# Performance work log

Hardware: AMD Instinct MI355X
Metric: run time of the kernel (lower is better)

The kernel has to match this reference:

```python
import jax, jax.numpy as jnp
import numpy as np

B, T, C = 2, 2048, 1024
H = 16
D = C // H  # 64
SCALE = 1.0 / np.sqrt(D)


def setup_inputs() -> dict:
    key = jax.random.key(0)
    k1, k2, k3 = jax.random.split(key, 3)
    x = jax.random.normal(k1, (B, T, C), dtype=jnp.float32)
    Wqkv = jax.random.normal(k2, (C, 3 * C), dtype=jnp.float32) * 0.02
    bqkv = jnp.zeros((3 * C,), dtype=jnp.float32)
    Wo = jax.random.normal(k3, (C, C), dtype=jnp.float32) * 0.02
    bo = jnp.zeros((C,), dtype=jnp.float32)
    return {"x": x, "Wqkv": Wqkv, "bqkv": bqkv, "Wo": Wo, "bo": bo}


def reference(x, Wqkv, bqkv, Wo, bo):
    Bsz, Tlen, Cdim = x.shape
    qkv = x @ Wqkv + bqkv                       # [B,T,3C]
    qkv = qkv.reshape(Bsz, Tlen, 3, H, D)
    qkv = jnp.transpose(qkv, (2, 0, 3, 1, 4))   # [3,B,H,T,D]
    q, k, v = qkv[0], qkv[1], qkv[2]
    att = jnp.einsum("bhqd,bhkd->bhqk", q, k) * SCALE
    # NOTE: faithful to source: mask keeps positions where k >= q
    i = jnp.arange(Tlen)
    mask = i[None, :] >= i[:, None]             # [T,T], entry [q,k]: k >= q
    att = jnp.where(mask[None, None], att, -jnp.inf)
    att = jax.nn.softmax(att, axis=-1)
    # dropout p=0.0 (inference) -> identity
    y = jnp.einsum("bhqk,bhkd->bhqd", att, v)   # [B,H,T,D]
    y = jnp.transpose(y, (0, 2, 1, 3)).reshape(Bsz, Tlen, Cdim)
    y = y @ Wo + bo
    return y
```

## Files before the change

kernel.cpp:

```cpp
#include <hip/hip_runtime.h>
#include <hip/hip_bf16.h>
#include <cstdint>
#include <cstddef>

typedef __bf16 bf16_t;
typedef __bf16 bf16x8 __attribute__((ext_vector_type(8)));
typedef __bf16 bf16x4 __attribute__((ext_vector_type(4)));
typedef short short4v __attribute__((ext_vector_type(4)));
typedef float f32x4 __attribute__((ext_vector_type(4)));

#define NB 2
#define NT 2048
#define NC 1024
#define NH 16
#define ND 64
#define NM (NB * NT)
#define N3 (3 * NC)
#define QSCALE_LOG2E 0.18033688011112042f

#define GLOAD_LDS16(gptr, lptr)                                                          \
  __builtin_amdgcn_global_load_lds((const __attribute__((address_space(1))) void*)(gptr), \
                                   (__attribute__((address_space(3))) void*)(lptr), 16, 0, 0)

__global__ __launch_bounds__(256) void prep_k(const float* __restrict__ x,
                                              const float* __restrict__ Wqkv,
                                              const float* __restrict__ Wo,
                                              bf16_t* __restrict__ xbf,
                                              bf16_t* __restrict__ wqkvT,
                                              bf16_t* __restrict__ woT) {
  __shared__ float tile[32][33];
  const int bx = blockIdx.x;
  if (bx < 4096) {
    const int i = (bx * 256 + threadIdx.x) * 4;
    const float4 v = *(const float4*)(x + i);
    bf16x4 o;
    o[0] = (bf16_t)v.x; o[1] = (bf16_t)v.y; o[2] = (bf16_t)v.z; o[3] = (bf16_t)v.w;
    *(bf16x4*)(xbf + i) = o;
    return;
  }
  const int t = bx - 4096;
  const int cxi = t & 127;
  const int tr = (t >> 7) * 32;
  const float* in;
  bf16_t* out;
  int Ccols, tc;
  if (cxi < 96) { in = Wqkv; out = wqkvT; Ccols = 3072; tc = cxi * 32; }
  else          { in = Wo;   out = woT;   Ccols = 1024; tc = (cxi - 96) * 32; }
  const int lx = threadIdx.x & 31;
  const int ly = threadIdx.x >> 5;
#pragma unroll
  for (int i = 0; i < 32; i += 8)
    tile[ly + i][lx] = in[(size_t)(tr + ly + i) * Ccols + tc + lx];
  __syncthreads();
#pragma unroll
  for (int i = 0; i < 32; i += 8)
    out[(size_t)(tc + ly + i) * 1024 + tr + lx] = (bf16_t)tile[lx][ly + i];
}

__global__ __launch_bounds__(256) void qkv_gemm_k(const bf16_t* __restrict__ A,
                                                  const bf16_t* __restrict__ Bt,
                                                  const float* __restrict__ bias,
                                                  bf16_t* __restrict__ qb,
                                                  bf16_t* __restrict__ kb,
                                                  bf16_t* __restrict__ vt2) {
  __shared__ __align__(16) bf16_t As0[4096], Bs0[4096], As1[4096], Bs1[4096];
  const int xcd = blockIdx.x & 7;
  const int i2 = blockIdx.x >> 3;
  const int m0 = (i2 & 31) * 128;
  const int n0 = (xcd * 3 + (i2 >> 5)) * 128;

  const int lane = threadIdx.x & 63;
  const int w = threadIdx.x >> 6;
  const int wm = (w & 1) * 64, wn = (w >> 1) * 64;
  const int quad = lane >> 4, l16 = lane & 15;

  f32x4 acc[4][4] = {};

  auto stage = [&](int k0, bf16_t* As_, bf16_t* Bs_) {
#pragma unroll
    for (int i = 0; i < 2; ++i) {
      const int gb = w * 128 + i * 64;
      const int g = gb + lane;
      GLOAD_LDS16(A + (size_t)(m0 + (g >> 2)) * NC + k0 + (g & 3) * 8, As_ + gb * 8);
      GLOAD_LDS16(Bt + (size_t)(n0 + (g >> 2)) * NC + k0 + (g & 3) * 8, Bs_ + gb * 8);
    }
  };

  auto compute = [&](const bf16_t* As_, const bf16_t* Bs_) {
    bf16x8 af[4], bfr[4];
#pragma unroll
    for (int i = 0; i < 4; ++i)
      af[i] = *(const bf16x8*)(As_ + (wm + i * 16 + l16) * 32 + quad * 8);
#pragma unroll
    for (int j = 0; j < 4; ++j)
      bfr[j] = *(const bf16x8*)(Bs_ + (wn + j * 16 + l16) * 32 + quad * 8);
#pragma unroll
    for (int i = 0; i < 4; ++i)
#pragma unroll
      for (int j = 0; j < 4; ++j)
        acc[i][j] = __builtin_amdgcn_mfma_f32_16x16x32_bf16(af[i], bfr[j], acc[i][j], 0, 0, 0);
  };

  stage(0, As0, Bs0);
  int k0 = 0;
  while (true) {
    __syncthreads();
    if (k0 + 32 < NC) stage(k0 + 32, As1, Bs1);
    compute(As0, Bs0);
    k0 += 32; if (k0 >= NC) break;
    __syncthreads();
    if (k0 + 32 < NC) stage(k0 + 32, As0, Bs0);
    compute(As1, Bs1);
    k0 += 32; if (k0 >= NC) break;
  }

#pragma unroll
  for (int i = 0; i < 4; ++i)
#pragma unroll
    for (int j = 0; j < 4; ++j) {
      const int n = n0 + wn + j * 16 + l16;
      const float bn = bias[n];
      const int which = n >> 10;
      const int rem = n & 1023;
      const int h = rem >> 6, d = rem & 63;
      const int mb = m0 + wm + i * 16 + quad * 4;
      const int b = mb >> 11, t4 = mb & 2047;
      const size_t bh = (size_t)b * NH + h;
      if (which == 2) {
        const int c = t4 >> 6, g = (t4 >> 2) & 15;
        bf16x4 val;
#pragma unroll
        for (int r = 0; r < 4; ++r) val[r] = (bf16_t)(acc[i][j][r] + bn);
        *(bf16x4*)(vt2 + ((bh * 32 + c) * 1024 + (size_t)g * 64 + d) * 4) = val;
      } else {
        bf16_t* dst = (which == 0) ? qb : kb;
        const float sc = (which == 0) ? QSCALE_LOG2E : 1.0f;
#pragma unroll
        for (int r = 0; r < 4; ++r)
          dst[(bh * NT + t4 + r) * ND + d] = (bf16_t)((acc[i][j][r] + bn) * sc);
      }
    }
}

__global__ __launch_bounds__(256, 4) void attn_k(const bf16_t* __restrict__ q,
                                                 const bf16_t* __restrict__ k,
                                                 const bf16_t* __restrict__ vt2,
                                                 bf16_t* __restrict__ y ) {
  const int bh = blockIdx.x & 31;
  const int u = (blockIdx.x >> 5) & 7;
  const int r4 = blockIdx.x >> 8;
  const int T = r4 * 8 + ((r4 & 1) ? (7 - u) : u);
  const int b = bh >> 4, h = bh & 15;

  const bf16_t* qp = q + (size_t)bh * NT * ND;
  const bf16_t* kp = k + (size_t)bh * NT * ND;
  const bf16_t* vp = vt2 + (size_t)bh * 32 * 4096;

  __shared__ __align__(16) bf16_t kbuf0[4096], kbuf1[4096];
  __shared__ __align__(16) bf16_t vbuf0[4096], vbuf1[4096];

  const int lane = threadIdx.x & 63;
  const int w = threadIdx.x >> 6;
  const int quad = lane >> 4, l16 = lane & 15;
  const int qv = T * 64 + w * 16 + l16;

  const bf16x8 qf0 = *(const bf16x8*)(qp + (size_t)qv * ND + quad * 8);
  const bf16x8 qf1 = *(const bf16x8*)(qp + (size_t)qv * ND + 32 + quad * 8);

  const short4v ones = {0x3F80, 0x3F80, 0x3F80, 0x3F80};

  f32x4 zs = {0.f, 0.f, 0.f, 0.f};
  f32x4 o[4];
#pragma unroll
  for (int dj = 0; dj < 4; ++dj) o[dj] = (f32x4){0.f, 0.f, 0.f, 0.f};

  auto stage = [&](int c, bf16_t* kb_, bf16_t* vb_) {
    const bf16_t* kc = kp + (size_t)c * 4096;
    const bf16_t* vc = vp + (size_t)c * 4096;
#pragma unroll
    for (int i = 0; i < 2; ++i) {
      const int gb = w * 128 + i * 64;
      const int s = gb + lane;
      const int row = s >> 3;
      const int cs = (s & 7) ^ (row & 7);
      GLOAD_LDS16(kc + (size_t)row * 64 + cs * 8, kb_ + gb * 8);
      GLOAD_LDS16(vc + (size_t)s * 8, vb_ + gb * 8);
    }
  };

  auto step = [&](const bf16_t* kt, const bf16_t* vt, int c) {
    const int t0 = c * 64;
    f32x4 sv[4];
#pragma unroll
    for (int kj = 0; kj < 4; ++kj) {
      const int kr = kj * 16 + l16;
      const int sw = kr & 7;
      const bf16x8 a0 = *(const bf16x8*)(kt + ((size_t)kr * 8 + (quad ^ sw)) * 8);
      const bf16x8 a1 = *(const bf16x8*)(kt + ((size_t)kr * 8 + ((4 + quad) ^ sw)) * 8);
      f32x4 z = {0.f, 0.f, 0.f, 0.f};
      z = __builtin_amdgcn_mfma_f32_16x16x32_bf16(a0, qf0, z, 0, 0, 0);
      z = __builtin_amdgcn_mfma_f32_16x16x32_bf16(a1, qf1, z, 0, 0, 0);
      sv[kj] = z;
    }
    if (c == T) {
#pragma unroll
      for (int kj = 0; kj < 4; ++kj)
#pragma unroll
        for (int r = 0; r < 4; ++r)
          if (t0 + kj * 16 + quad * 4 + r < qv) sv[kj][r] = -INFINITY;
    }
    short4v pf[4];
#pragma unroll
    for (int kj = 0; kj < 4; ++kj) {
      bf16x4 pb;
#pragma unroll
      for (int r = 0; r < 4; ++r) pb[r] = (bf16_t)__builtin_amdgcn_exp2f(sv[kj][r]);
      pf[kj] = __builtin_bit_cast(short4v, pb);
    }
#pragma unroll
    for (int kj = 0; kj < 4; ++kj)
      zs = __builtin_amdgcn_mfma_f32_16x16x16bf16_1k(ones, pf[kj], zs, 0, 0, 0);
#pragma unroll
    for (int dj = 0; dj < 4; ++dj) {
#pragma unroll
      for (int kj = 0; kj < 4; ++kj) {
        const bf16x4 a =
            *(const bf16x4*)(vt + ((size_t)(kj * 4 + quad) * 64 + dj * 16 + l16) * 4);
        o[dj] = __builtin_amdgcn_mfma_f32_16x16x16bf16_1k(
            __builtin_bit_cast(short4v, a), pf[kj], o[dj], 0, 0, 0);
      }
    }
  };

  stage(T, kbuf0, vbuf0);
  int c = T;
  while (true) {
    __syncthreads();
    if (c + 1 < 32) stage(c + 1, kbuf1, vbuf1);
    step(kbuf0, vbuf0, c);
    if (++c >= 32) break;
    __syncthreads();
    if (c + 1 < 32) stage(c + 1, kbuf0, vbuf0);
    step(kbuf1, vbuf1, c);
    if (++c >= 32) break;
  }

  const float inv = 1.0f / zs[0];
  const size_t base = ((size_t)b * NT + qv) * NC + h * 64;
#pragma unroll
  for (int dj = 0; dj < 4; ++dj) {
    bf16x4 va;
#pragma unroll
    for (int r = 0; r < 4; ++r) va[r] = (bf16_t)(o[dj][r] * inv);
    *(bf16x4*)(y + base + dj * 16 + quad * 4) = va;
  }
}

__global__ __launch_bounds__(256) void out_gemm_k(const bf16_t* __restrict__ A,
                                                  const bf16_t* __restrict__ Bt,
                                                  const float* __restrict__ bias,
                                                  float* __restrict__ out) {
  __shared__ __align__(16) bf16_t lds[6144];
  bf16_t* As = lds;
  bf16_t* Bs = lds + 2048;
  const int n0 = (blockIdx.x & 7) * 128;
  const int m0 = (blockIdx.x >> 3) * 64;

  const int lane = threadIdx.x & 63;
  const int w = threadIdx.x >> 6;
  const int wm = (w & 1) * 32, wn = (w >> 1) * 64;
  const int quad = lane >> 4, l16 = lane & 15;

  f32x4 acc[2][4] = {};

  for (int k0 = 0; k0 < NC; k0 += 32) {
    {
      const int g = w * 64 + lane;
      GLOAD_LDS16(A + (size_t)(m0 + (g >> 2)) * NC + k0 + (g & 3) * 8, As + w * 64 * 8);
    }
#pragma unroll
    for (int i = 0; i < 2; ++i) {
      const int gb = w * 128 + i * 64;
      const int g = gb + lane;
      GLOAD_LDS16(Bt + (size_t)(n0 + (g >> 2)) * NC + k0 + (g & 3) * 8, Bs + gb * 8);
    }
    __syncthreads();
    bf16x8 af[2], bfr[4];
#pragma unroll
    for (int i = 0; i < 2; ++i)
      af[i] = *(const bf16x8*)(As + ((wm + i * 16 + l16) * 4 + quad) * 8);
#pragma unroll
    for (int j = 0; j < 4; ++j)
      bfr[j] = *(const bf16x8*)(Bs + ((wn + j * 16 + l16) * 4 + quad) * 8);
#pragma unroll
    for (int i = 0; i < 2; ++i)
#pragma unroll
      for (int j = 0; j < 4; ++j)
        acc[i][j] = __builtin_amdgcn_mfma_f32_16x16x32_bf16(af[i], bfr[j], acc[i][j], 0, 0, 0);
    __syncthreads();
  }

#pragma unroll
  for (int i = 0; i < 2; ++i)
#pragma unroll
    for (int j = 0; j < 4; ++j) {
      const int n = n0 + wn + j * 16 + l16;
      const float bn = bias[n];
#pragma unroll
      for (int r = 0; r < 4; ++r) {
        const int m = m0 + wm + i * 16 + quad * 4 + r;
        out[(size_t)m * NC + n] = acc[i][j][r] + bn;
      }
    }
}

extern "C" void kernel_launch(void* const* d_in, const int* in_sizes, int n_in,
                              void* d_out, int out_size, void* d_ws, size_t ws_size,
                              hipStream_t stream) {
  const float* x = (const float*)d_in[0];
  const float* Wqkv = (const float*)d_in[1];
  const float* bqkv = (const float*)d_in[2];
  const float* Wo = (const float*)d_in[3];
  const float* bo = (const float*)d_in[4];
  float* out = (float*)d_out;

  char* p = (char*)d_ws;
  bf16_t* xbf = (bf16_t*)p;   p += (size_t)NM * NC * sizeof(bf16_t);
  bf16_t* wqkvT = (bf16_t*)p; p += (size_t)N3 * NC * sizeof(bf16_t);
  bf16_t* woT = (bf16_t*)p;   p += (size_t)NC * NC * sizeof(bf16_t);
  bf16_t* qb = (bf16_t*)p;    p += (size_t)NB * NH * NT * ND * sizeof(bf16_t);
  bf16_t* kb = (bf16_t*)p;    p += (size_t)NB * NH * NT * ND * sizeof(bf16_t);
  bf16_t* vt2 = (bf16_t*)p;   p += (size_t)NB * NH * NT * ND * sizeof(bf16_t);
  bf16_t* yb = (bf16_t*)p;    p += (size_t)NM * NC * sizeof(bf16_t);

  hipLaunchKernelGGL(prep_k, dim3(8192), dim3(256), 0, stream,
                     x, Wqkv, Wo, xbf, wqkvT, woT);
  hipLaunchKernelGGL(qkv_gemm_k, dim3(768), dim3(256), 0, stream,
                     xbf, wqkvT, bqkv, qb, kb, vt2);
  hipLaunchKernelGGL(attn_k, dim3(1024), dim3(256), 0, stream, qb, kb, vt2, yb);
  hipLaunchKernelGGL(out_gemm_k, dim3(512), dim3(256), 0, stream,
                     yb, woT, bo, out);
}
```

Measured before the change: 164.1 us.

## Process two query subtiles per wave in attention, halving block size

The attention kernel now runs 2 waves per block instead of 4. Each wave handles 32 query rows as two 16-row subtiles, so every K and V fragment read from LDS feeds twice as many MFMAs. Each thread stages twice as many K/V chunks into LDS. This cuts LDS read traffic and barrier cost per unit of work, in exchange for more registers per wave and fewer waves to hide latency.

Measured after the change: 181.5 us. 1.11x slower.

```diff
diff --git a/kernel.cpp b/kernel.cpp
--- a/kernel.cpp
+++ b/kernel.cpp
@@ -142,7 +142,7 @@
     }
 }
 
-__global__ __launch_bounds__(256, 4) void attn_k(const bf16_t* __restrict__ q,
+__global__ __launch_bounds__(128, 2) void attn_k(const bf16_t* __restrict__ q,
                                                  const bf16_t* __restrict__ k,
                                                  const bf16_t* __restrict__ vt2,
                                                  bf16_t* __restrict__ y ) {
@@ -162,24 +162,34 @@
   const int lane = threadIdx.x & 63;
   const int w = threadIdx.x >> 6;
   const int quad = lane >> 4, l16 = lane & 15;
-  const int qv = T * 64 + w * 16 + l16;
-
-  const bf16x8 qf0 = *(const bf16x8*)(qp + (size_t)qv * ND + quad * 8);
-  const bf16x8 qf1 = *(const bf16x8*)(qp + (size_t)qv * ND + 32 + quad * 8);
+  const int qv0 = T * 64 + w * 32 + l16;
+  const int qv1 = qv0 + 16;
+
+  bf16x8 qf[2][2];
+#pragma unroll
+  for (int s = 0; s < 2; ++s) {
+    const int qv = qv0 + s * 16;
+    qf[s][0] = *(const bf16x8*)(qp + (size_t)qv * ND + quad * 8);
+    qf[s][1] = *(const bf16x8*)(qp + (size_t)qv * ND + 32 + quad * 8);
+  }
 
   const short4v ones = {0x3F80, 0x3F80, 0x3F80, 0x3F80};
 
-  f32x4 zs = {0.f, 0.f, 0.f, 0.f};
-  f32x4 o[4];
-#pragma unroll
-  for (int dj = 0; dj < 4; ++dj) o[dj] = (f32x4){0.f, 0.f, 0.f, 0.f};
+  f32x4 zs[2];
+  f32x4 o[2][4];
+#pragma unroll
+  for (int s = 0; s < 2; ++s) {
+    zs[s] = (f32x4){0.f, 0.f, 0.f, 0.f};
+#pragma unroll
+    for (int dj = 0; dj < 4; ++dj) o[s][dj] = (f32x4){0.f, 0.f, 0.f, 0.f};
+  }
 
   auto stage = [&](int c, bf16_t* kb_, bf16_t* vb_) {
     const bf16_t* kc = kp + (size_t)c * 4096;
     const bf16_t* vc = vp + (size_t)c * 4096;
 #pragma unroll
-    for (int i = 0; i < 2; ++i) {
-      const int gb = w * 128 + i * 64;
+    for (int i = 0; i < 4; ++i) {
+      const int gb = w * 256 + i * 64;
       const int s = gb + lane;
       const int row = s >> 3;
       const int cs = (s & 7) ^ (row & 7);
@@ -190,44 +200,55 @@
 
   auto step = [&](const bf16_t* kt, const bf16_t* vt, int c) {
     const int t0 = c * 64;
-    f32x4 sv[4];
+    f32x4 sv[2][4];
 #pragma unroll
     for (int kj = 0; kj < 4; ++kj) {
       const int kr = kj * 16 + l16;
       const int sw = kr & 7;
       const bf16x8 a0 = *(const bf16x8*)(kt + ((size_t)kr * 8 + (quad ^ sw)) * 8);
       const bf16x8 a1 = *(const bf16x8*)(kt + ((size_t)kr * 8 + ((4 + quad) ^ sw)) * 8);
-      f32x4 z = {0.f, 0.f, 0.f, 0.f};
-      z = __builtin_amdgcn_mfma_f32_16x16x32_bf16(a0, qf0, z, 0, 0, 0);
-      z = __builtin_amdgcn_mfma_f32_16x16x32_bf16(a1, qf1, z, 0, 0, 0);
-      sv[kj] = z;
+#pragma unroll
+      for (int s = 0; s < 2; ++s) {
+        f32x4 z = {0.f, 0.f, 0.f, 0.f};
+        z = __builtin_amdgcn_mfma_f32_16x16x32_bf16(a0, qf[s][0], z, 0, 0, 0);
+        z = __builtin_amdgcn_mfma_f32_16x16x32_bf16(a1, qf[s][1], z, 0, 0, 0);
+        sv[s][kj] = z;
+      }
     }
     if (c == T) {
 #pragma unroll
+      for (int s = 0; s < 2; ++s)
+#pragma unroll
+        for (int kj = 0; kj < 4; ++kj)
+#pragma unroll
+          for (int r = 0; r < 4; ++r)
+            if (t0 + kj * 16 + quad * 4 + r < qv0 + s * 16) sv[s][kj][r] = -INFINITY;
+    }
+    short4v pf[2][4];
+#pragma unroll
+    for (int s = 0; s < 2; ++s)
+#pragma unroll
+      for (int kj = 0; kj < 4; ++kj) {
+        bf16x4 pb;
+#pragma unroll
+        for (int r = 0; r < 4; ++r) pb[r] = (bf16_t)__builtin_amdgcn_exp2f(sv[s][kj][r]);
+        pf[s][kj] = __builtin_bit_cast(short4v, pb);
+      }
+#pragma unroll
+    for (int s = 0; s < 2; ++s)
+#pragma unroll
       for (int kj = 0; kj < 4; ++kj)
-#pragma unroll
-        for (int r = 0; r < 4; ++r)
-          if (t0 + kj * 16 + quad * 4 + r < qv) sv[kj][r] = -INFINITY;
-    }
-    short4v pf[4];
-#pragma unroll
-    for (int kj = 0; kj < 4; ++kj) {
-      bf16x4 pb;
-#pragma unroll
-      for (int r = 0; r < 4; ++r) pb[r] = (bf16_t)__builtin_amdgcn_exp2f(sv[kj][r]);
-      pf[kj] = __builtin_bit_cast(short4v, pb);
-    }
-#pragma unroll
-    for (int kj = 0; kj < 4; ++kj)
-      zs = __builtin_amdgcn_mfma_f32_16x16x16bf16_1k(ones, pf[kj], zs, 0, 0, 0);
+        zs[s] = __builtin_amdgcn_mfma_f32_16x16x16bf16_1k(ones, pf[s][kj], zs[s], 0, 0, 0);
 #pragma unroll
     for (int dj = 0; dj < 4; ++dj) {
 #pragma unroll
       for (int kj = 0; kj < 4; ++kj) {
         const bf16x4 a =
             *(const bf16x4*)(vt + ((size_t)(kj * 4 + quad) * 64 + dj * 16 + l16) * 4);
-        o[dj] = __builtin_amdgcn_mfma_f32_16x16x16bf16_1k(
-            __builtin_bit_cast(short4v, a), pf[kj], o[dj], 0, 0, 0);
+        const short4v vfs = __builtin_bit_cast(short4v, a);
+#pragma unroll
+        for (int s = 0; s < 2; ++s)
+          o[s][dj] = __builtin_amdgcn_mfma_f32_16x16x16bf16_1k(vfs, pf[s][kj], o[s][dj], 0, 0, 0);
       }
     }
   };
@@ -245,14 +266,17 @@
     if (++c >= 32) break;
   }
 
-  const float inv = 1.0f / zs[0];
-  const size_t base = ((size_t)b * NT + qv) * NC + h * 64;
-#pragma unroll
-  for (int dj = 0; dj < 4; ++dj) {
-    bf16x4 va;
-#pragma unroll
-    for (int r = 0; r < 4; ++r) va[r] = (bf16_t)(o[dj][r] * inv);
-    *(bf16x4*)(y + base + dj * 16 + quad * 4) = va;
+#pragma unroll
+  for (int s = 0; s < 2; ++s) {
+    const float inv = 1.0f / zs[s][0];
+    const size_t base = ((size_t)b * NT + qv0 + s * 16) * NC + h * 64;
+#pragma unroll
+    for (int dj = 0; dj < 4; ++dj) {
+      bf16x4 va;
+#pragma unroll
+      for (int r = 0; r < 4; ++r) va[r] = (bf16_t)(o[s][dj][r] * inv);
+      *(bf16x4*)(y + base + dj * 16 + quad * 4) = va;
+    }
   }
 }
 
@@ -337,7 +361,7 @@
                      x, Wqkv, Wo, xbf, wqkvT, woT);
   hipLaunchKernelGGL(qkv_gemm_k, dim3(768), dim3(256), 0, stream,
                      xbf, wqkvT, bqkv, qb, kb, vt2);
-  hipLaunchKernelGGL(attn_k, dim3(1024), dim3(256), 0, stream, qb, kb, vt2, yb);
+  hipLaunchKernelGGL(attn_k, dim3(1024), dim3(128), 0, stream, qb, kb, vt2, yb);
   hipLaunchKernelGGL(out_gemm_k, dim3(512), dim3(256), 0, stream,
                      yb, woT, bo, out);
 }
```
